# Kernel optimization log

Measured on AMD Instinct MI355X. Metric: run time of the kernel, lower is better.

The kernel has to match this reference:

```python
import jax, jax.numpy as jnp
import numpy as np

B, T, H, E = 128, 512, 512, 512
V_IN, V_OUT = 50000, 30000


def setup_inputs() -> dict:
    key = jax.random.key(0)
    ks = jax.random.split(key, 24)
    f = jax.random.normal
    stdv = 1.0 / np.sqrt(H)
    return {
        "inputs": jax.random.randint(ks[0], (B,), 0, V_IN),
        "last_hidden": f(ks[1], (1, B, H), dtype=jnp.float32),
        "code_outputs": f(ks[2], (T, B, H), dtype=jnp.float32),
        "ast_outputs": f(ks[3], (T, B, H), dtype=jnp.float32),
        "code_coverage": jax.random.uniform(ks[4], (B, T), dtype=jnp.float32),
        "ast_coverage": jax.random.uniform(ks[5], (B, T), dtype=jnp.float32),
        "embedding": f(ks[6], (V_IN, E)) * 0.01,
        "code_W_attn": f(ks[7], (H, 3 * H)) * 0.02,
        "code_b_attn": f(ks[8], (H,)) * 0.01,
        "code_v": f(ks[9], (H,)) * stdv,
        "code_W_cov": f(ks[10], (H,)) * 0.02,
        "ast_W_attn": f(ks[11], (H, 3 * H)) * 0.02,
        "ast_b_attn": f(ks[12], (H,)) * 0.01,
        "ast_v": f(ks[13], (H,)) * stdv,
        "ast_W_cov": f(ks[14], (H,)) * 0.02,
        "gru_W_ih": f(ks[15], (3 * H, E + H)) * 0.02,
        "gru_W_hh": f(ks[16], (3 * H, H)) * 0.02,
        "gru_b_ih": f(ks[17], (3 * H,)) * 0.01,
        "gru_b_hh": f(ks[18], (3 * H,)) * 0.01,
        "W_out": f(ks[19], (V_OUT, 2 * H)) * 0.01,
        "b_out": f(ks[20], (V_OUT,)) * 0.01,
    }


def _attention(hidden, enc, cov, W, b, v, Wc):
    # hidden [B,H], enc [T,B,H], cov [B,T]; Wc is the [H] weight of Linear(1,H,bias=False)
    encb = jnp.swapaxes(enc, 0, 1)  # [B,T,H]
    h = jnp.broadcast_to(hidden[:, None, :], encb.shape)  # [B,T,H]
    cov_feat = cov[:, :, None] * Wc  # [B,T,H]
    feat = jnp.concatenate([h, encb, cov_feat], axis=2)  # [B,T,3H]
    energy = jax.nn.relu(feat @ W.T + b)  # [B,T,H]
    scores = energy @ v  # [B,T]
    w = jax.nn.softmax(scores, axis=1)  # softmax over T
    return w, cov + w


def reference(inputs, last_hidden, code_outputs, ast_outputs, code_coverage,
              ast_coverage, embedding, code_W_attn, code_b_attn, code_v,
              code_W_cov, ast_W_attn, ast_b_attn, ast_v, ast_W_cov,
              gru_W_ih, gru_W_hh, gru_b_ih, gru_b_hh, W_out, b_out):
    h0 = last_hidden[0]  # [B,H]
    emb = embedding[inputs]  # [B,E]

    cw, ccov = _attention(h0, code_outputs, code_coverage,
                          code_W_attn, code_b_attn, code_v, code_W_cov)
    aw, acov = _attention(h0, ast_outputs, ast_coverage,
                          ast_W_attn, ast_b_attn, ast_v, ast_W_cov)

    code_ctx = jnp.einsum('bt,tbh->bh', cw, code_outputs)
    ast_ctx = jnp.einsum('bt,tbh->bh', aw, ast_outputs)
    ctx = 0.5 * (code_ctx + ast_ctx)  # [B,H]

    # one-step GRU (PyTorch gate layout: r, z, n)
    x = jnp.concatenate([emb, ctx], axis=1)  # [B,E+H]
    gi = x @ gru_W_ih.T + gru_b_ih
    gh = h0 @ gru_W_hh.T + gru_b_hh
    i_r, i_z, i_n = jnp.split(gi, 3, axis=1)
    h_r, h_z, h_n = jnp.split(gh, 3, axis=1)
    r = jax.nn.sigmoid(i_r + h_r)
    z = jax.nn.sigmoid(i_z + h_z)
    n = jnp.tanh(i_n + r * h_n)
    h1 = (1.0 - z) * n + z * h0  # [B,H]

    logits = jnp.concatenate([h1, ctx], axis=1) @ W_out.T + b_out  # [B,V_OUT]
    out = jax.nn.log_softmax(logits, axis=1)
    return (out, h1[None], cw[:, None, :], aw[:, None, :], ccov, acov)
```

## Files before the change

### kernel.cpp

```cpp
#include <hip/hip_runtime.h>
#include <math.h>

#define B_ 128
#define T_ 512
#define H_ 512
#define E_ 512
#define VOUT 30000
#define M_ (T_*B_)

typedef __attribute__((ext_vector_type(8))) short short8;
typedef __attribute__((ext_vector_type(4))) float f32x4;

__device__ __forceinline__ short8 cvt8v(float4 a, float4 b) {
    unsigned int r0, r1, r2, r3;
    asm("v_cvt_pk_bf16_f32 %0, %1, %2" : "=v"(r0) : "v"(a.x), "v"(a.y));
    asm("v_cvt_pk_bf16_f32 %0, %1, %2" : "=v"(r1) : "v"(a.z), "v"(a.w));
    asm("v_cvt_pk_bf16_f32 %0, %1, %2" : "=v"(r2) : "v"(b.x), "v"(b.y));
    asm("v_cvt_pk_bf16_f32 %0, %1, %2" : "=v"(r3) : "v"(b.z), "v"(b.w));
    union { unsigned int u[4]; short8 s; } u;
    u.u[0] = r0; u.u[1] = r1; u.u[2] = r2; u.u[3] = r3;
    return u.s;
}
__device__ __forceinline__ short8 cvt8(const float* p) {
    return cvt8v(*(const float4*)p, *(const float4*)(p + 4));
}


__global__ void emb_gather(const int* idx, const float* emb, float* x) {
    int b = blockIdx.x; int t = threadIdx.x;
    int row = idx[b];
    x[b*1024 + t]       = emb[(size_t)row*E_ + t];
    x[b*1024 + t + 256] = emb[(size_t)row*E_ + t + 256];
}

__global__ void prep_a1(const float* h0, const float* Wc, const float* bc_,
                        const float* Wa, const float* ba, float* A1) {
    int hc = blockIdx.x;
    int bcb = blockIdx.y;
    int which = blockIdx.z;
    const float* W    = which ? Wa : Wc;
    const float* bias = which ? ba : bc_;
    int b0 = bcb * 16;
    int tid = threadIdx.x;
    __shared__ float hs[16][512];
    for (int idx = tid; idx < 2048; idx += 256) {
        int row = idx >> 7, c = (idx & 127) * 4;
        *(float4*)&hs[row][c] = *(const float4*)(h0 + (size_t)(b0+row)*512 + c);
    }
    __syncthreads();
    int h = hc*64 + (tid & 63);
    int r = (tid >> 6) * 4;
    const float* Wr = W + (size_t)h * 1536;
    float a0=0.f, a1=0.f, a2=0.f, a3=0.f;
    for (int k = 0; k < 512; k += 4) {
        float4 w  = *(const float4*)(Wr + k);
        float4 x0 = *(const float4*)&hs[r][k];
        float4 x1 = *(const float4*)&hs[r+1][k];
        float4 x2 = *(const float4*)&hs[r+2][k];
        float4 x3 = *(const float4*)&hs[r+3][k];
        a0 += w.x*x0.x + w.y*x0.y + w.z*x0.z + w.w*x0.w;
        a1 += w.x*x1.x + w.y*x1.y + w.z*x1.z + w.w*x1.w;
        a2 += w.x*x2.x + w.y*x2.y + w.z*x2.z + w.w*x2.w;
        a3 += w.x*x3.x + w.y*x3.y + w.z*x3.z + w.w*x3.w;
    }
    float bb = bias[h];
    A1[((size_t)which*B_ + (b0+r  ))*H_ + h] = a0 + bb;
    A1[((size_t)which*B_ + (b0+r+1))*H_ + h] = a1 + bb;
    A1[((size_t)which*B_ + (b0+r+2))*H_ + h] = a2 + bb;
    A1[((size_t)which*B_ + (b0+r+3))*H_ + h] = a3 + bb;
}

__global__ void prep_u(const float* wcov_c, const float* W_c,
                       const float* wcov_a, const float* W_a, float* u) {
    int which = blockIdx.x; int h = threadIdx.x;
    const float* W  = which ? W_a : W_c;
    const float* wc = which ? wcov_a : wcov_c;
    const float* Wr = W + (size_t)h*1536 + 1024;
    float s = 0.f;
    for (int k = 0; k < H_; ++k) s += wc[k] * Wr[k];
    u[which*H_ + h] = s;
}


#define BK 64
#define LDSS 72

__global__ __launch_bounds__(1024)
void attn_gemm(const float* code_enc, const float* ast_enc,
               const float* code_W, const float* ast_W,
               const float* code_v, const float* ast_v,
               const float* code_cov, const float* ast_cov,
               const float* A1, const float* u, float* scores) {
    int which = blockIdx.y;
    const float* enc = which ? ast_enc : code_enc;
    const float* W   = which ? ast_W   : code_W;
    const float* vv  = which ? ast_v   : code_v;
    const float* cov = which ? ast_cov : code_cov;
    const float* A1w = A1 + (size_t)which * B_ * H_;
    const float* uw  = u + which * H_;
    float* sc = scores + (size_t)which * M_;

    int bid = blockIdx.x;
    int mt  = ((bid & 7) << 6) + (bid >> 3);
    int m0  = mt * 128;

    __shared__ __align__(16) ushort As[128 * LDSS];
    __shared__ __align__(16) ushort Bs[512 * LDSS];
    __shared__ float red[128][8];

    int tid = threadIdx.x;
    int lane = tid & 63, wave = tid >> 6;
    int wm2 = wave >> 3, wn8 = wave & 7;
    int col = lane & 15, quad = lane >> 4;

    int arow = tid >> 3, ac8 = (tid & 7) * 8;
    const float* asrc = enc + (size_t)(m0 + arow) * H_ + ac8;
    const float* bsrc = W + (size_t)arow * 1536 + 512 + ac8;

    f32x4 acc[4][4];
    #pragma unroll
    for (int i = 0; i < 4; ++i)
        #pragma unroll
        for (int j = 0; j < 4; ++j) acc[i][j] = (f32x4)(0.f);

    float4 ra0, ra1, rb[8];
    ra0 = *(const float4*)(asrc);
    ra1 = *(const float4*)(asrc + 4);
    #pragma unroll
    for (int it = 0; it < 4; ++it) {
        const float* p = bsrc + (size_t)it * 196608;
        rb[2*it]   = *(const float4*)(p);
        rb[2*it+1] = *(const float4*)(p + 4);
    }

    for (int kt = 0; kt < 8; ++kt) {
        __syncthreads();
        *(short8*)(&As[arow * LDSS + ac8]) = cvt8v(ra0, ra1);
        #pragma unroll
        for (int it = 0; it < 4; ++it)
            *(short8*)(&Bs[(it*128 + arow) * LDSS + ac8]) = cvt8v(rb[2*it], rb[2*it+1]);
        __syncthreads();
        if (kt < 7) {
            int k0 = (kt + 1) * BK;
            ra0 = *(const float4*)(asrc + k0);
            ra1 = *(const float4*)(asrc + k0 + 4);
            #pragma unroll
            for (int it = 0; it < 4; ++it) {
                const float* p = bsrc + (size_t)it * 196608 + k0;
                rb[2*it]   = *(const float4*)(p);
                rb[2*it+1] = *(const float4*)(p + 4);
            }
        }
        #pragma unroll
        for (int kk = 0; kk < BK; kk += 32) {
            short8 af[4], bfr[4];
            #pragma unroll
            for (int i = 0; i < 4; ++i)
                af[i] = *(const short8*)(&As[(wm2*64 + i*16 + col) * LDSS + kk + quad*8]);
            #pragma unroll
            for (int j = 0; j < 4; ++j)
                bfr[j] = *(const short8*)(&Bs[(wn8*64 + j*16 + col) * LDSS + kk + quad*8]);
            #pragma unroll
            for (int i = 0; i < 4; ++i)
                #pragma unroll
                for (int j = 0; j < 4; ++j)
                    acc[i][j] = __builtin_amdgcn_mfma_f32_16x16x32_bf16(af[i], bfr[j], acc[i][j], 0, 0, 0);
        }
    }

    float u4[4], v4[4]; int h4[4];
    #pragma unroll
    for (int j = 0; j < 4; ++j) {
        int h = wn8*64 + j*16 + col;
        h4[j] = h; u4[j] = uw[h]; v4[j] = vv[h];
    }
    #pragma unroll
    for (int i = 0; i < 4; ++i) {
        #pragma unroll
        for (int r = 0; r < 4; ++r) {
            int b = wm2*64 + i*16 + quad*4 + r;
            float cv = cov[b*T_ + mt];
            float s = 0.f;
            #pragma unroll
            for (int j = 0; j < 4; ++j) {
                float val = acc[i][j][r] + A1w[b*H_ + h4[j]] + cv * u4[j];
                val = val > 0.f ? val : 0.f;
                s += val * v4[j];
            }
            #pragma unroll
            for (int off = 1; off < 16; off <<= 1) s += __shfl_xor(s, off, 64);
            if (col == 0) red[b][wn8] = s;
        }
    }
    __syncthreads();
    if (tid < 128) {
        float s = 0.f;
        #pragma unroll
        for (int w = 0; w < 8; ++w) s += red[tid][w];
        sc[(size_t)tid * T_ + mt] = s;
    }
}

__global__ void attn_softmax(const float* scores, const float* code_cov, const float* ast_cov,
                             float* wsm, float* out) {
    int b = blockIdx.x, which = blockIdx.y;
    const float* sc = scores + (size_t)which * M_ + (size_t)b * T_;
    const float* cov = which ? ast_cov : code_cov;
    float* wrow = wsm + ((size_t)which * B_ + b) * T_;
    float* w_out   = out + 3840000 + 65536 + (size_t)which * 65536 + b * T_;
    float* cov_out = out + 3840000 + 65536 + 131072 + (size_t)which * 65536 + b * T_;
    int tid = threadIdx.x;
    __shared__ float red[8];
    float v0 = sc[tid];
    float v1 = sc[tid + 256];
    float m = fmaxf(v0, v1);
    #pragma unroll
    for (int off = 32; off; off >>= 1) m = fmaxf(m, __shfl_xor(m, off, 64));
    if ((tid & 63) == 0) red[tid >> 6] = m;
    __syncthreads();
    m = fmaxf(fmaxf(red[0], red[1]), fmaxf(red[2], red[3]));
    float e0 = expf(v0 - m), e1 = expf(v1 - m);
    float s = e0 + e1;
    #pragma unroll
    for (int off = 32; off; off >>= 1) s += __shfl_xor(s, off, 64);
    if ((tid & 63) == 0) red[4 + (tid >> 6)] = s;
    __syncthreads();
    float inv = 1.f / (red[4] + red[5] + red[6] + red[7]);
    float w0 = e0 * inv, w1 = e1 * inv;
    wrow[tid] = w0; wrow[tid + 256] = w1;
    w_out[tid] = w0; w_out[tid + 256] = w1;
    cov_out[tid]       = cov[b*T_ + tid]       + w0;
    cov_out[tid + 256] = cov[b*T_ + tid + 256] + w1;
}

__global__ void ctx_kernel(const float* code_enc, const float* ast_enc,
                           const float* wsm, float* x) {
    int b = blockIdx.x, tc = blockIdx.y;
    int tid = threadIdx.x;
    __shared__ float wc[64], wa[64];
    if (tid < 64) {
        wc[tid] = wsm[(size_t)b * T_ + tc*64 + tid];
        wa[tid] = wsm[(size_t)(B_ + b) * T_ + tc*64 + tid];
    }
    __syncthreads();
    float a0=0.f, a1=0.f, a2=0.f, a3=0.f;
    for (int i = 0; i < 64; ++i) {
        int t = tc * 64 + i;
        float4 c4 = *(const float4*)(code_enc + (size_t)t * (B_*H_) + b*H_ + tid*4);
        float4 a4 = *(const float4*)(ast_enc  + (size_t)t * (B_*H_) + b*H_ + tid*4);
        a0 += wc[i]*c4.x + wa[i]*a4.x;
        a1 += wc[i]*c4.y + wa[i]*a4.y;
        a2 += wc[i]*c4.z + wa[i]*a4.z;
        a3 += wc[i]*c4.w + wa[i]*a4.w;
    }
    atomicAdd(&x[b*1024 + 512 + tid*4],     0.5f*a0);
    atomicAdd(&x[b*1024 + 512 + tid*4 + 1], 0.5f*a1);
    atomicAdd(&x[b*1024 + 512 + tid*4 + 2], 0.5f*a2);
    atomicAdd(&x[b*1024 + 512 + tid*4 + 3], 0.5f*a3);
}

__global__ void gru_gemm(const float* x, const float* h0, const float* Wih, const float* Whh,
                         const float* bih, const float* bhh, float* g) {
    int nc = blockIdx.x;
    int bcb = blockIdx.y;
    int b0 = bcb * 8;
    int tid = threadIdx.x;
    __shared__ float xs[8][1024];
    __shared__ float hs[8][512];
    for (int idx = tid; idx < 2048; idx += 256) {
        int row = idx >> 8, c = (idx & 255) * 4;
        *(float4*)&xs[row][c] = *(const float4*)(x + (size_t)(b0+row)*1024 + c);
    }
    for (int idx = tid; idx < 1024; idx += 256) {
        int row = idx >> 7, c = (idx & 127) * 4;
        *(float4*)&hs[row][c] = *(const float4*)(h0 + (size_t)(b0+row)*512 + c);
    }
    __syncthreads();
    int n = nc * 64 + (tid & 63);
    int r0 = (tid >> 6) * 2, r1 = r0 + 1;
    const float* wi = Wih + (size_t)n * 1024;
    const float* wh = Whh + (size_t)n * 512;
    float si0=0.f, si1=0.f, sh0=0.f, sh1=0.f;
    for (int k = 0; k < 1024; k += 4) {
        float4 w  = *(const float4*)(wi + k);
        float4 x0 = *(const float4*)&xs[r0][k];
        float4 x1 = *(const float4*)&xs[r1][k];
        si0 += w.x*x0.x + w.y*x0.y + w.z*x0.z + w.w*x0.w;
        si1 += w.x*x1.x + w.y*x1.y + w.z*x1.z + w.w*x1.w;
    }
    for (int k = 0; k < 512; k += 4) {
        float4 w  = *(const float4*)(wh + k);
        float4 x0 = *(const float4*)&hs[r0][k];
        float4 x1 = *(const float4*)&hs[r1][k];
        sh0 += w.x*x0.x + w.y*x0.y + w.z*x0.z + w.w*x0.w;
        sh1 += w.x*x1.x + w.y*x1.y + w.z*x1.z + w.w*x1.w;
    }
    int gate = n >> 9, h = n & 511;
    float bi = bih[n], bh = bhh[n];
    int b;
    b = b0 + r0;
    {
        float A = si0 + bi, Bv = sh0 + bh;
        if (gate == 0)      g[b*512 + h] = A + Bv;
        else if (gate == 1) g[65536 + b*512 + h] = A + Bv;
        else { g[131072 + b*512 + h] = A; g[196608 + b*512 + h] = Bv; }
    }
    b = b0 + r1;
    {
        float A = si1 + bi, Bv = sh1 + bh;
        if (gate == 0)      g[b*512 + h] = A + Bv;
        else if (gate == 1) g[65536 + b*512 + h] = A + Bv;
        else { g[131072 + b*512 + h] = A; g[196608 + b*512 + h] = Bv; }
    }
}

__global__ void gru_finish(const float* g, const float* x, const float* h0,
                           float* out, float* y) {
    int i = blockIdx.x * 256 + threadIdx.x;
    int b = i >> 9, h = i & 511;
    float r = 1.f / (1.f + expf(-g[i]));
    float z = 1.f / (1.f + expf(-g[65536 + i]));
    float nn = tanhf(g[131072 + i] + r * g[196608 + i]);
    float h1 = (1.f - z) * nn + z * h0[i];
    out[3840000 + i] = h1;
    y[b*1024 + h]       = h1;
    y[b*1024 + 512 + h] = x[b*1024 + 512 + h];
}

__global__ __launch_bounds__(256)
void logits_gemm(const float* y, const float* Wout, const float* bout, float* out0) {
    int n0 = blockIdx.x * 128;
    __shared__ __align__(16) ushort As[128 * LDSS];
    __shared__ __align__(16) ushort Bs[128 * LDSS];
    int tid = threadIdx.x, lane = tid & 63, wave = tid >> 6;
    int wm = wave >> 1, wn = wave & 1;
    int col = lane & 15, quad = lane >> 4;
    f32x4 acc[4][4];
    #pragma unroll
    for (int i = 0; i < 4; ++i)
        #pragma unroll
        for (int j = 0; j < 4; ++j) acc[i][j] = (f32x4)(0.f);

    for (int k0 = 0; k0 < 1024; k0 += BK) {
        __syncthreads();
        #pragma unroll
        for (int it = 0; it < 4; ++it) {
            int c = it * 256 + tid;
            int row = c >> 3, c8 = (c & 7) * 8;
            *(short8*)(&As[row * LDSS + c8]) =
                cvt8(y + (size_t)row * 1024 + k0 + c8);
            int brow = n0 + row; if (brow > VOUT-1) brow = VOUT-1;
            *(short8*)(&Bs[row * LDSS + c8]) =
                cvt8(Wout + (size_t)brow * 1024 + k0 + c8);
        }
        __syncthreads();
        #pragma unroll
        for (int kk = 0; kk < BK; kk += 32) {
            short8 af[4], bfr[4];
            #pragma unroll
            for (int i = 0; i < 4; ++i)
                af[i] = *(const short8*)(&As[(wm*64 + i*16 + col) * LDSS + kk + quad*8]);
            #pragma unroll
            for (int j = 0; j < 4; ++j)
                bfr[j] = *(const short8*)(&Bs[(wn*64 + j*16 + col) * LDSS + kk + quad*8]);
            #pragma unroll
            for (int i = 0; i < 4; ++i)
                #pragma unroll
                for (int j = 0; j < 4; ++j)
                    acc[i][j] = __builtin_amdgcn_mfma_f32_16x16x32_bf16(af[i], bfr[j], acc[i][j], 0, 0, 0);
        }
    }
    #pragma unroll
    for (int i = 0; i < 4; ++i)
        #pragma unroll
        for (int j = 0; j < 4; ++j) {
            int h = n0 + wn*64 + j*16 + col;
            if (h < VOUT) {
                float bo = bout[h];
                #pragma unroll
                for (int r = 0; r < 4; ++r) {
                    int m = wm*64 + i*16 + quad*4 + r;
                    out0[(size_t)m * VOUT + h] = acc[i][j][r] + bo;
                }
            }
        }
}

__global__ void logsoftmax(float* out0) {
    int b = blockIdx.x; int tid = threadIdx.x;
    float* row = out0 + (size_t)b * VOUT;
    __shared__ float red[8];
    float m = -1e30f;
    for (int i = tid; i < VOUT; i += 256) m = fmaxf(m, row[i]);
    #pragma unroll
    for (int off = 32; off; off >>= 1) m = fmaxf(m, __shfl_xor(m, off, 64));
    if ((tid & 63) == 0) red[tid >> 6] = m;
    __syncthreads();
    m = fmaxf(fmaxf(red[0], red[1]), fmaxf(red[2], red[3]));
    float s = 0.f;
    for (int i = tid; i < VOUT; i += 256) s += expf(row[i] - m);
    #pragma unroll
    for (int off = 32; off; off >>= 1) s += __shfl_xor(s, off, 64);
    if ((tid & 63) == 0) red[4 + (tid >> 6)] = s;
    __syncthreads();
    float lse = m + logf(red[4] + red[5] + red[6] + red[7]);
    for (int i = tid; i < VOUT; i += 256) row[i] = row[i] - lse;
}

extern "C" void kernel_launch(void* const* d_in, const int* in_sizes, int n_in,
                              void* d_out, int out_size, void* d_ws, size_t ws_size,
                              hipStream_t stream) {
    const int*   inputs   = (const int*)d_in[0];
    const float* h0       = (const float*)d_in[1];
    const float* code_enc = (const float*)d_in[2];
    const float* ast_enc  = (const float*)d_in[3];
    const float* code_cov = (const float*)d_in[4];
    const float* ast_cov  = (const float*)d_in[5];
    const float* emb      = (const float*)d_in[6];
    const float* code_W   = (const float*)d_in[7];
    const float* code_b   = (const float*)d_in[8];
    const float* code_v   = (const float*)d_in[9];
    const float* code_Wc  = (const float*)d_in[10];
    const float* ast_W    = (const float*)d_in[11];
    const float* ast_b    = (const float*)d_in[12];
    const float* ast_v    = (const float*)d_in[13];
    const float* ast_Wc   = (const float*)d_in[14];
    const float* gru_Wih  = (const float*)d_in[15];
    const float* gru_Whh  = (const float*)d_in[16];
    const float* gru_bih  = (const float*)d_in[17];
    const float* gru_bhh  = (const float*)d_in[18];
    const float* W_out    = (const float*)d_in[19];
    const float* b_out    = (const float*)d_in[20];
    float* out = (float*)d_out;

    char* ws = (char*)d_ws;
    float* scores = (float*)(ws + 0);
    float* x      = (float*)(ws + 524288);
    float* A1     = (float*)(ws + 1048576);
    float* wsm    = (float*)(ws + 1572864);
    float* u      = (float*)(ws + 2097152);
    float* g      = (float*)(ws + 2101248);
    float* y      = (float*)(ws + 3149824);

    hipMemsetAsync(ws + 524288, 0, 524288, stream);

    emb_gather<<<dim3(B_), dim3(256), 0, stream>>>(inputs, emb, x);
    prep_a1<<<dim3(8, 8, 2), dim3(256), 0, stream>>>(h0, code_W, code_b, ast_W, ast_b, A1);
    prep_u<<<dim3(2), dim3(512), 0, stream>>>(code_Wc, code_W, ast_Wc, ast_W, u);

    attn_gemm<<<dim3(512, 2), dim3(1024), 0, stream>>>(
        code_enc, ast_enc, code_W, ast_W, code_v, ast_v, code_cov, ast_cov, A1, u, scores);

    attn_softmax<<<dim3(B_, 2), dim3(256), 0, stream>>>(scores, code_cov, ast_cov, wsm, out);

    ctx_kernel<<<dim3(B_, 8), dim3(128), 0, stream>>>(code_enc, ast_enc, wsm, x);

    gru_gemm<<<dim3(24, 16), dim3(256), 0, stream>>>(x, h0, gru_Wih, gru_Whh, gru_bih, gru_bhh, g);
    gru_finish<<<dim3(256), dim3(256), 0, stream>>>(g, x, h0, out, y);

    logits_gemm<<<dim3(235), dim3(256), 0, stream>>>(y, W_out, b_out, out);
    logsoftmax<<<dim3(B_), dim3(256), 0, stream>>>(out);
}
```

Measured before the change: 857.7 us.

## Double-buffer LDS tiles with BK=32 in attention and logits GEMMs

Both bf16 MFMA GEMMs switch from a single 64-wide K tile to two ping-pong 32-wide LDS buffers. This removes one __syncthreads per K step and overlaps the global prefetch of the next tile with MFMA on the current one. The logits GEMM also gains register prefetching, where before it loaded and converted its tiles synchronously. The cost is more loop iterations and twice as many barriers relative to K, and the LDS row padding changes to 40 halfwords, which may alter bank conflicts.

```diff
diff --git a/kernel.cpp b/kernel.cpp
--- a/kernel.cpp
+++ b/kernel.cpp
@@ -20,9 +20,6 @@
     union { unsigned int u[4]; short8 s; } u;
     u.u[0] = r0; u.u[1] = r1; u.u[2] = r2; u.u[3] = r3;
     return u.s;
-}
-__device__ __forceinline__ short8 cvt8(const float* p) {
-    return cvt8v(*(const float4*)p, *(const float4*)(p + 4));
 }
 
 
@@ -82,8 +79,7 @@
 }
 
 
-#define BK 64
-#define LDSS 72
+#define ALS 40
 
 __global__ __launch_bounds__(1024)
 void attn_gemm(const float* code_enc, const float* ast_enc,
@@ -104,8 +100,8 @@
     int mt  = ((bid & 7) << 6) + (bid >> 3);
     int m0  = mt * 128;
 
-    __shared__ __align__(16) ushort As[128 * LDSS];
-    __shared__ __align__(16) ushort Bs[512 * LDSS];
+    __shared__ __align__(16) ushort As[2][128 * ALS];
+    __shared__ __align__(16) ushort Bs[2][512 * ALS];
     __shared__ float red[128][8];
 
     int tid = threadIdx.x;
@@ -113,9 +109,14 @@
     int wm2 = wave >> 3, wn8 = wave & 7;
     int col = lane & 15, quad = lane >> 4;
 
-    int arow = tid >> 3, ac8 = (tid & 7) * 8;
-    const float* asrc = enc + (size_t)(m0 + arow) * H_ + ac8;
-    const float* bsrc = W + (size_t)arow * 1536 + 512 + ac8;
+    int srow = tid >> 2, sc8 = (tid & 3) * 8;
+    const float* asrc  = enc + (size_t)(m0 + srow) * H_ + sc8;
+    const float* bsrc0 = W + (size_t)srow * 1536 + 512 + sc8;
+    const float* bsrc1 = W + (size_t)(256 + srow) * 1536 + 512 + sc8;
+    ushort* adst = &As[0][srow * ALS + sc8];
+    ushort* bdst0 = &Bs[0][srow * ALS + sc8];
+    ushort* bdst1 = &Bs[0][(256 + srow) * ALS + sc8];
+    const int bufstep_a = 128 * ALS, bufstep_b = 512 * ALS;
 
     f32x4 acc[4][4];
     #pragma unroll
@@ -123,49 +124,35 @@
         #pragma unroll
         for (int j = 0; j < 4; ++j) acc[i][j] = (f32x4)(0.f);
 
-    float4 ra0, ra1, rb[8];
-    ra0 = *(const float4*)(asrc);
-    ra1 = *(const float4*)(asrc + 4);
-    #pragma unroll
-    for (int it = 0; it < 4; ++it) {
-        const float* p = bsrc + (size_t)it * 196608;
-        rb[2*it]   = *(const float4*)(p);
-        rb[2*it+1] = *(const float4*)(p + 4);
-    }
-
-    for (int kt = 0; kt < 8; ++kt) {
+    float4 ra0, ra1, rb0a, rb0b, rb1a, rb1b;
+    if (tid < 512) { ra0 = *(const float4*)(asrc); ra1 = *(const float4*)(asrc + 4); }
+    rb0a = *(const float4*)(bsrc0); rb0b = *(const float4*)(bsrc0 + 4);
+    rb1a = *(const float4*)(bsrc1); rb1b = *(const float4*)(bsrc1 + 4);
+
+    for (int kt = 0; kt < 16; ++kt) {
+        int cur = kt & 1;
+        if (tid < 512) *(short8*)(adst + cur * bufstep_a) = cvt8v(ra0, ra1);
+        *(short8*)(bdst0 + cur * bufstep_b) = cvt8v(rb0a, rb0b);
+        *(short8*)(bdst1 + cur * bufstep_b) = cvt8v(rb1a, rb1b);
         __syncthreads();
-        *(short8*)(&As[arow * LDSS + ac8]) = cvt8v(ra0, ra1);
-        #pragma unroll
-        for (int it = 0; it < 4; ++it)
-            *(short8*)(&Bs[(it*128 + arow) * LDSS + ac8]) = cvt8v(rb[2*it], rb[2*it+1]);
-        __syncthreads();
-        if (kt < 7) {
-            int k0 = (kt + 1) * BK;
-            ra0 = *(const float4*)(asrc + k0);
-            ra1 = *(const float4*)(asrc + k0 + 4);
-            #pragma unroll
-            for (int it = 0; it < 4; ++it) {
-                const float* p = bsrc + (size_t)it * 196608 + k0;
-                rb[2*it]   = *(const float4*)(p);
-                rb[2*it+1] = *(const float4*)(p + 4);
-            }
+        if (kt < 15) {
+            int k0 = (kt + 1) * 32;
+            if (tid < 512) { ra0 = *(const float4*)(asrc + k0); ra1 = *(const float4*)(asrc + k0 + 4); }
+            rb0a = *(const float4*)(bsrc0 + k0); rb0b = *(const float4*)(bsrc0 + k0 + 4);
+            rb1a = *(const float4*)(bsrc1 + k0); rb1b = *(const float4*)(bsrc1 + k0 + 4);
         }
-        #pragma unroll
-        for (int kk = 0; kk < BK; kk += 32) {
-            short8 af[4], bfr[4];
-            #pragma unroll
-            for (int i = 0; i < 4; ++i)
-                af[i] = *(const short8*)(&As[(wm2*64 + i*16 + col) * LDSS + kk + quad*8]);
+        short8 af[4], bfr[4];
+        #pragma unroll
+        for (int i = 0; i < 4; ++i)
+            af[i] = *(const short8*)(&As[cur][(wm2*64 + i*16 + col) * ALS + quad*8]);
+        #pragma unroll
+        for (int j = 0; j < 4; ++j)
+            bfr[j] = *(const short8*)(&Bs[cur][(wn8*64 + j*16 + col) * ALS + quad*8]);
+        #pragma unroll
+        for (int i = 0; i < 4; ++i)
             #pragma unroll
             for (int j = 0; j < 4; ++j)
-                bfr[j] = *(const short8*)(&Bs[(wn8*64 + j*16 + col) * LDSS + kk + quad*8]);
-            #pragma unroll
-            for (int i = 0; i < 4; ++i)
-                #pragma unroll
-                for (int j = 0; j < 4; ++j)
-                    acc[i][j] = __builtin_amdgcn_mfma_f32_16x16x32_bf16(af[i], bfr[j], acc[i][j], 0, 0, 0);
-        }
+                acc[i][j] = __builtin_amdgcn_mfma_f32_16x16x32_bf16(af[i], bfr[j], acc[i][j], 0, 0, 0);
     }
 
     float u4[4], v4[4]; int h4[4];
@@ -330,8 +317,8 @@
 __global__ __launch_bounds__(256)
 void logits_gemm(const float* y, const float* Wout, const float* bout, float* out0) {
     int n0 = blockIdx.x * 128;
-    __shared__ __align__(16) ushort As[128 * LDSS];
-    __shared__ __align__(16) ushort Bs[128 * LDSS];
+    __shared__ __align__(16) ushort As[2][128 * ALS];
+    __shared__ __align__(16) ushort Bs[2][128 * ALS];
     int tid = threadIdx.x, lane = tid & 63, wave = tid >> 6;
     int wm = wave >> 1, wn = wave & 1;
     int col = lane & 15, quad = lane >> 4;
@@ -341,34 +328,51 @@
         #pragma unroll
         for (int j = 0; j < 4; ++j) acc[i][j] = (f32x4)(0.f);
 
-    for (int k0 = 0; k0 < 1024; k0 += BK) {
+    int srow = tid >> 2, sc8 = (tid & 3) * 8;
+    int br0 = n0 + srow;       if (br0 > VOUT-1) br0 = VOUT-1;
+    int br1 = n0 + 64 + srow;  if (br1 > VOUT-1) br1 = VOUT-1;
+    const float* asrc0 = y + (size_t)srow * 1024 + sc8;
+    const float* asrc1 = y + (size_t)(64 + srow) * 1024 + sc8;
+    const float* bsrc0 = Wout + (size_t)br0 * 1024 + sc8;
+    const float* bsrc1 = Wout + (size_t)br1 * 1024 + sc8;
+    ushort* adst0 = &As[0][srow * ALS + sc8];
+    ushort* adst1 = &As[0][(64 + srow) * ALS + sc8];
+    ushort* bdst0 = &Bs[0][srow * ALS + sc8];
+    ushort* bdst1 = &Bs[0][(64 + srow) * ALS + sc8];
+    const int bufstep = 128 * ALS;
+
+    float4 ya0a, ya0b, ya1a, ya1b, wb0a, wb0b, wb1a, wb1b;
+    ya0a = *(const float4*)(asrc0); ya0b = *(const float4*)(asrc0 + 4);
+    ya1a = *(const float4*)(asrc1); ya1b = *(const float4*)(asrc1 + 4);
+    wb0a = *(const float4*)(bsrc0); wb0b = *(const float4*)(bsrc0 + 4);
+    wb1a = *(const float4*)(bsrc1); wb1b = *(const float4*)(bsrc1 + 4);
+
+    for (int kt = 0; kt < 32; ++kt) {
+        int cur = kt & 1;
+        *(short8*)(adst0 + cur * bufstep) = cvt8v(ya0a, ya0b);
+        *(short8*)(adst1 + cur * bufstep) = cvt8v(ya1a, ya1b);
+        *(short8*)(bdst0 + cur * bufstep) = cvt8v(wb0a, wb0b);
+        *(short8*)(bdst1 + cur * bufstep) = cvt8v(wb1a, wb1b);
         __syncthreads();
-        #pragma unroll
-        for (int it = 0; it < 4; ++it) {
-            int c = it * 256 + tid;
-            int row = c >> 3, c8 = (c & 7) * 8;
-            *(short8*)(&As[row * LDSS + c8]) =
-                cvt8(y + (size_t)row * 1024 + k0 + c8);
-            int brow = n0 + row; if (brow > VOUT-1) brow = VOUT-1;
-            *(short8*)(&Bs[row * LDSS + c8]) =
-                cvt8(Wout + (size_t)brow * 1024 + k0 + c8);
+        if (kt < 31) {
+            int k0 = (kt + 1) * 32;
+            ya0a = *(const float4*)(asrc0 + k0); ya0b = *(const float4*)(asrc0 + k0 + 4);
+            ya1a = *(const float4*)(asrc1 + k0); ya1b = *(const float4*)(asrc1 + k0 + 4);
+            wb0a = *(const float4*)(bsrc0 + k0); wb0b = *(const float4*)(bsrc0 + k0 + 4);
+            wb1a = *(const float4*)(bsrc1 + k0); wb1b = *(const float4*)(bsrc1 + k0 + 4);
         }
-        __syncthreads();
-        #pragma unroll
-        for (int kk = 0; kk < BK; kk += 32) {
-            short8 af[4], bfr[4];
-            #pragma unroll
-            for (int i = 0; i < 4; ++i)
-                af[i] = *(const short8*)(&As[(wm*64 + i*16 + col) * LDSS + kk + quad*8]);
+        short8 af[4], bfr[4];
+        #pragma unroll
+        for (int i = 0; i < 4; ++i)
+            af[i] = *(const short8*)(&As[cur][(wm*64 + i*16 + col) * ALS + quad*8]);
+        #pragma unroll
+        for (int j = 0; j < 4; ++j)
+            bfr[j] = *(const short8*)(&Bs[cur][(wn*64 + j*16 + col) * ALS + quad*8]);
+        #pragma unroll
+        for (int i = 0; i < 4; ++i)
             #pragma unroll
             for (int j = 0; j < 4; ++j)
-                bfr[j] = *(const short8*)(&Bs[(wn*64 + j*16 + col) * LDSS + kk + quad*8]);
-            #pragma unroll
-            for (int i = 0; i < 4; ++i)
-                #pragma unroll
-                for (int j = 0; j < 4; ++j)
-                    acc[i][j] = __builtin_amdgcn_mfma_f32_16x16x32_bf16(af[i], bfr[j], acc[i][j], 0, 0, 0);
-        }
+                acc[i][j] = __builtin_amdgcn_mfma_f32_16x16x32_bf16(af[i], bfr[j], acc[i][j], 0, 0, 0);
     }
     #pragma unroll
     for (int i = 0; i < 4; ++i)
```

Result: faster. 824.6 us (-3.9%).
